# Optimization experiments

Hardware: AMD Instinct MI355X
Metric: run time of the kernel (lower is better)

The kernel has to match this reference:

```python
import jax, jax.numpy as jnp
import numpy as np

V = 12000; WE = 1000; FEAT = 2048; FE = 1024; H = 1024; AH = 512; NREG = 36; B = 128; T = 17
PAD_ID = 0


def _lstm_cell(x, h, c, wih, whh, bih, bhh):
    # torch LSTMCell: gates ordered (input, forget, cell, output)
    g = x @ wih.T + h @ whh.T + bih + bhh
    i, f, gg, o = jnp.split(g, 4, axis=-1)
    c_new = jax.nn.sigmoid(f) * c + jax.nn.sigmoid(i) * jnp.tanh(gg)
    h_new = jax.nn.sigmoid(o) * jnp.tanh(c_new)
    return h_new, c_new


def setup_inputs() -> dict:
    key = jax.random.key(0)
    ks = jax.random.split(key, 24)
    s = 0.02
    emb_w = jax.random.normal(ks[0], (V, WE), jnp.float32) * s
    emb_w = emb_w.at[PAD_ID].set(0.0)  # padding_idx row is zero
    inp = {
        'fc_feats': jax.random.normal(ks[1], (B, FEAT), jnp.float32),
        'att_feats': jax.random.normal(ks[2], (B, NREG, FEAT), jnp.float32),
        'captions': jax.random.randint(ks[3], (B, T), 0, V, jnp.int64),
        'emb_w': emb_w,
        'fc_w': jax.random.normal(ks[4], (FEAT, FE), jnp.float32) * s,
        'fc_b': jnp.zeros((FE,), jnp.float32),
        'atte_w': jax.random.normal(ks[5], (FEAT, FE), jnp.float32) * s,
        'atte_b': jnp.zeros((FE,), jnp.float32),
        'ctx_w': jax.random.normal(ks[6], (FE, AH), jnp.float32) * s,
        'ctx_b': jnp.zeros((AH,), jnp.float32),
        'attl_wih': jax.random.normal(ks[7], (4 * H, H + FE + WE), jnp.float32) * s,
        'attl_whh': jax.random.normal(ks[8], (4 * H, H), jnp.float32) * s,
        'attl_bih': jnp.zeros((4 * H,), jnp.float32),
        'attl_bhh': jnp.zeros((4 * H,), jnp.float32),
        'h2att_w': jax.random.normal(ks[9], (H, AH), jnp.float32) * s,
        'h2att_b': jnp.zeros((AH,), jnp.float32),
        'alpha_w': jax.random.normal(ks[10], (AH,), jnp.float32) * s,
        'alpha_b': jnp.zeros((), jnp.float32),
        'langl_wih': jax.random.normal(ks[11], (4 * H, FE + H), jnp.float32) * s,
        'langl_whh': jax.random.normal(ks[12], (4 * H, H), jnp.float32) * s,
        'langl_bih': jnp.zeros((4 * H,), jnp.float32),
        'langl_bhh': jnp.zeros((4 * H,), jnp.float32),
        'cls_w': jax.random.normal(ks[13], (H, V), jnp.float32) * s,
        'cls_b': jnp.zeros((V,), jnp.float32),
    }
    return inp


def _forward(fc_feats, att_feats, captions, emb_w, fc_w, fc_b, atte_w, atte_b,
             ctx_w, ctx_b, attl_wih, attl_whh, attl_bih, attl_bhh,
             h2att_w, h2att_b, alpha_w, alpha_b,
             langl_wih, langl_whh, langl_bih, langl_bhh, cls_w, cls_b):
    # _prepare_features (eval mode: dropout is identity)
    fc_e = jax.nn.relu(fc_feats @ fc_w + fc_b)                 # [B, FE]
    att_e = jax.nn.relu(att_feats @ atte_w + atte_b)           # [B, N, FE]
    p_att = att_e @ ctx_w + ctx_b                              # [B, N, AH]
    bsz = fc_feats.shape[0]
    h0 = jnp.zeros((bsz, H), fc_feats.dtype)

    def step(carry, it):
        h_att, c_att, h_lang, c_lang = carry
        w = jax.nn.relu(emb_w[it])                             # [B, WE]
        x_att = jnp.concatenate([h_lang, fc_e, w], axis=1)
        h_att, c_att = _lstm_cell(x_att, h_att, c_att, attl_wih, attl_whh, attl_bih, attl_bhh)
        # Attention
        hq = h_att @ h2att_w + h2att_b                          # [B, AH]
        e = jnp.tanh(p_att + hq[:, None, :]) @ alpha_w + alpha_b  # [B, N]
        alpha = jax.nn.softmax(e, axis=1)
        att_res = jnp.einsum('bn,bnd->bd', alpha, att_e)        # [B, FE]
        x_lang = jnp.concatenate([att_res, h_att], axis=1)
        h_lang, c_lang = _lstm_cell(x_lang, h_lang, c_lang, langl_wih, langl_whh, langl_bih, langl_bhh)
        logprobs = jax.nn.log_softmax(h_lang @ cls_w + cls_b, axis=1)  # [B, V]
        return (h_att, c_att, h_lang, c_lang), logprobs

    its = captions[:, :-1].T  # [T-1, B]
    _, outs = jax.lax.scan(step, (h0, h0, h0, h0), its)
    return jnp.transpose(outs, (1, 0, 2))  # [B, T-1, V]


def reference(fc_feats, att_feats, captions, emb_w, fc_w, fc_b, atte_w, atte_b,
              ctx_w, ctx_b, attl_wih, attl_whh, attl_bih, attl_bhh,
              h2att_w, h2att_b, alpha_w, alpha_b,
              langl_wih, langl_whh, langl_bih, langl_bhh, cls_w, cls_b):
    return _forward(fc_feats, att_feats, captions, emb_w, fc_w, fc_b, atte_w, atte_b,
                    ctx_w, ctx_b, attl_wih, attl_whh, attl_bih, attl_bhh,
                    h2att_w, h2att_b, alpha_w, alpha_b,
                    langl_wih, langl_whh, langl_bih, langl_bhh, cls_w, cls_b)
```

## Files before the change

kernel.cpp:

```cpp
#include <hip/hip_runtime.h>
#include <cstddef>
#include <cstdint>

constexpr int CV    = 12000;
constexpr int CVP2  = 12288;
constexpr int CWE   = 1000;
constexpr int CFEAT = 2048;
constexpr int CFE   = 1024;
constexpr int CH    = 1024;
constexpr int CAH   = 512;
constexpr int CNREG = 36;
constexpr int CB    = 128;
constexpr int CT    = 17;
constexpr int G4    = 4096;
constexpr int XH    = 2048;
constexpr int XL3   = 3072;

#define CDIV(a,b) (((a)+(b)-1)/(b))

typedef __bf16 bf16_t;
typedef __bf16 bf16x8 __attribute__((ext_vector_type(8)));
typedef __bf16 bf16x4 __attribute__((ext_vector_type(4)));
typedef float  f32x4  __attribute__((ext_vector_type(4)));

typedef __attribute__((address_space(3))) uint32_t lds_u32;
typedef const __attribute__((address_space(1))) uint32_t glb_u32;

struct Seg { const bf16_t* A; const bf16_t* W; int lda, ldw, kt; };

template<bool RELU, bool OUTBF, int SWZ>
__global__ __launch_bounds__(256)
void pre_gemm(Seg s0, int inner, const float* __restrict__ bias1,
              void* __restrict__ Cout, int ldc)
{
    const int tid = threadIdx.x;
    const int wid = tid >> 6, lane = tid & 63;
    const int wr = wid >> 1, wc = wid & 1;
    const int llo = lane & 15, lhi = lane >> 4;
    const int nb = gridDim.x, id = blockIdx.x;
    const int sw = (id & 7) * (nb >> 3) + (id >> 3);
    int m0, n0;
    if (SWZ == 1)      { n0 = (sw / inner) * 64;  m0 = (sw % inner) * 128; }
    else if (SWZ == 2) { m0 = (sw / inner) * 128; n0 = (sw % inner) * 64;  }
    else {
        const int xcd = id & 7, idx = id >> 3;
        m0 = (((xcd >> 2) << 3) + (idx & 7)) * 128;
        n0 = (((xcd & 3) << 4) + (idx >> 3)) * 64;
    }

    __shared__ __align__(16) uint8_t sm[2][24576];

    const int TT = s0.kt;
    f32x4 acc[4][2] = {};
    uint4 ra[4], rb[2];
    const int srow = tid >> 3, sc = tid & 7;
    const int cswz = (sc ^ (srow & 7)) << 4;

    auto load_tile = [&](int ti) {
        const int k0 = ti << 6;
        #pragma unroll
        for (int i = 0; i < 4; ++i)
            ra[i] = *(const uint4*)(s0.A + (size_t)(m0 + i * 32 + srow) * s0.lda + k0 + sc * 8);
        #pragma unroll
        for (int i = 0; i < 2; ++i)
            rb[i] = *(const uint4*)(s0.W + (size_t)(n0 + i * 32 + srow) * s0.ldw + k0 + sc * 8);
    };
    auto write_tile = [&](int buf) {
        uint8_t* base = sm[buf];
        #pragma unroll
        for (int i = 0; i < 4; ++i) *(uint4*)(base + (i * 32 + srow) * 128 + cswz) = ra[i];
        #pragma unroll
        for (int i = 0; i < 2; ++i) *(uint4*)(base + 16384 + (i * 32 + srow) * 128 + cswz) = rb[i];
    };
    auto compute = [&](int buf) {
        const uint8_t* base = sm[buf];
        const int r7 = llo & 7;
        #pragma unroll
        for (int kk = 0; kk < 2; ++kk) {
            const int coff = ((kk * 4 + lhi) ^ r7) << 4;
            bf16x8 af[4], bg[2];
            #pragma unroll
            for (int fm = 0; fm < 4; ++fm)
                af[fm] = *(const bf16x8*)(base + (wr * 64 + fm * 16 + llo) * 128 + coff);
            #pragma unroll
            for (int fn = 0; fn < 2; ++fn)
                bg[fn] = *(const bf16x8*)(base + 16384 + (wc * 32 + fn * 16 + llo) * 128 + coff);
            #pragma unroll
            for (int fm = 0; fm < 4; ++fm)
                #pragma unroll
                for (int fn = 0; fn < 2; ++fn)
                    acc[fm][fn] = __builtin_amdgcn_mfma_f32_16x16x32_bf16(
                        af[fm], bg[fn], acc[fm][fn], 0, 0, 0);
        }
    };

    load_tile(0); write_tile(0);
    load_tile(1);
    __syncthreads();
    int cur = 0;
    for (int ti = 0; ti < TT; ++ti) {
        if (ti + 1 < TT) write_tile(cur ^ 1);
        if (ti + 2 < TT) load_tile(ti + 2);
        compute(cur);
        __syncthreads();
        cur ^= 1;
    }

    if (OUTBF) {
        bf16_t* st = (bf16_t*)sm[0];
        #pragma unroll
        for (int fn = 0; fn < 2; ++fn) {
            const int lcol = wc * 32 + fn * 16 + llo;
            const float b = bias1 ? bias1[n0 + lcol] : 0.f;
            #pragma unroll
            for (int fm = 0; fm < 4; ++fm)
                #pragma unroll
                for (int r = 0; r < 4; ++r) {
                    float v = acc[fm][fn][r] + b;
                    if (RELU) v = fmaxf(v, 0.f);
                    st[(wr * 64 + fm * 16 + lhi * 4 + r) * 64 + lcol] = (bf16_t)v;
                }
        }
        __syncthreads();
        #pragma unroll
        for (int i = 0; i < 4; ++i) {
            const int q = tid + i * 256;
            const int row = q >> 3, ch = q & 7;
            *(uint4*)((bf16_t*)Cout + (size_t)(m0 + row) * ldc + n0 + ch * 8)
                = *(const uint4*)&st[row * 64 + ch * 8];
        }
    } else {
        const int colb = n0 + wc * 32;
        const int rowb = m0 + wr * 64 + lhi * 4;
        #pragma unroll
        for (int fn = 0; fn < 2; ++fn) {
            const int col = colb + fn * 16 + llo;
            const float b = bias1 ? bias1[col] : 0.f;
            #pragma unroll
            for (int fm = 0; fm < 4; ++fm)
                #pragma unroll
                for (int r = 0; r < 4; ++r) {
                    float v = acc[fm][fn][r] + b;
                    if (RELU) v = fmaxf(v, 0.f);
                    ((float*)Cout)[(size_t)(rowb + fm * 16 + r) * ldc + col] = v;
                }
        }
    }
}

__global__ __launch_bounds__(256)
void cls_gemm(const bf16_t* __restrict__ A, const bf16_t* __restrict__ W,
              const float* __restrict__ bias, bf16_t* __restrict__ Cout)
{
    const int tid = threadIdx.x;
    const int wid = tid >> 6, lane = tid & 63;
    const int wr = wid >> 1, wc = wid & 1;
    const int llo = lane & 15, lhi = lane >> 4;
    const int id = blockIdx.x;
    const int xcd = id & 7, idx = id >> 3;
    const int mg = xcd & 1, ng = xcd >> 1;
    const int m0 = (mg * 8 + (idx & 7)) * 128;
    const int n0 = (ng * 24 + (idx >> 3)) * 128;

    __shared__ __align__(16) uint8_t pool[65536];
    auto bufA = [&](int b) { return pool + b * 16384; };
    auto bufB = [&](int b) { return pool + 32768 + b * 16384; };

    constexpr int TT = 16;
    f32x4 acc[4][4] = {};
    uint4 ra[4], rbv[4];

    auto load_tile = [&](int ti) {
        const int k0 = ti << 6;
        #pragma unroll
        for (int i = 0; i < 4; ++i) {
            const int q = tid + i * 256;
            const int row = q >> 3, c = q & 7;
            ra[i]  = *(const uint4*)(A + (size_t)(m0 + row) * CH + k0 + c * 8);
            rbv[i] = *(const uint4*)(W + (size_t)(n0 + row) * CH + k0 + c * 8);
        }
    };
    auto write_tile = [&](int buf) {
        #pragma unroll
        for (int i = 0; i < 4; ++i) {
            const int q = tid + i * 256;
            const int row = q >> 3, c = q & 7;
            const int o = row * 128 + ((c ^ (row & 7)) << 4);
            *(uint4*)(bufA(buf) + o) = ra[i];
            *(uint4*)(bufB(buf) + o) = rbv[i];
        }
    };
    auto compute = [&](int buf) {
        const int r7 = llo & 7;
        #pragma unroll
        for (int kk = 0; kk < 2; ++kk) {
            const int coff = ((kk * 4 + lhi) ^ r7) << 4;
            bf16x8 af[4], bg[4];
            #pragma unroll
            for (int fm = 0; fm < 4; ++fm)
                af[fm] = *(const bf16x8*)(bufA(buf) + (wr * 64 + fm * 16 + llo) * 128 + coff);
            #pragma unroll
            for (int fn = 0; fn < 4; ++fn)
                bg[fn] = *(const bf16x8*)(bufB(buf) + (wc * 64 + fn * 16 + llo) * 128 + coff);
            #pragma unroll
            for (int fm = 0; fm < 4; ++fm)
                #pragma unroll
                for (int fn = 0; fn < 4; ++fn)
                    acc[fm][fn] = __builtin_amdgcn_mfma_f32_16x16x32_bf16(
                        af[fm], bg[fn], acc[fm][fn], 0, 0, 0);
        }
    };

    load_tile(0); write_tile(0);
    load_tile(1);
    __syncthreads();
    int cur = 0;
    for (int ti = 0; ti < TT; ++ti) {
        if (ti + 1 < TT) write_tile(cur ^ 1);
        if (ti + 2 < TT) load_tile(ti + 2);
        compute(cur);
        __syncthreads();
        cur ^= 1;
    }

    bf16_t* st = (bf16_t*)pool;
    #pragma unroll
    for (int fn = 0; fn < 4; ++fn) {
        const int lcol = wc * 64 + fn * 16 + llo;
        const int col = n0 + lcol;
        const float b = (col < CV) ? bias[col] : 0.f;
        #pragma unroll
        for (int fm = 0; fm < 4; ++fm)
            #pragma unroll
            for (int r = 0; r < 4; ++r)
                st[(wr * 64 + fm * 16 + lhi * 4 + r) * 128 + lcol]
                    = (bf16_t)(acc[fm][fn][r] + b);
    }
    __syncthreads();
    #pragma unroll
    for (int i = 0; i < 8; ++i) {
        const int q = tid + i * 256;
        const int row = q >> 4, ch = q & 15;
        *(uint4*)(Cout + (size_t)(m0 + row) * CVP2 + n0 + ch * 8)
            = *(const uint4*)&st[row * 128 + ch * 8];
    }
}

template<int TAG>
__global__ __launch_bounds__(256)
void gate_split(const bf16_t* __restrict__ A, int lda,
                const bf16_t* __restrict__ W, int ldw, int ktz,
                bf16_t* __restrict__ gpart)
{
    const int tid = threadIdx.x;
    const int w = tid >> 6, lane = tid & 63;
    const int llo = lane & 15, lhi = lane >> 4;
    const int n0 = blockIdx.x * 16;
    const int z  = blockIdx.y;
    const int kb = z * ktz;

    __shared__ __align__(16) uint8_t smA[2][16384];
    __shared__ __align__(16) uint8_t smB[2][2048];

    f32x4 acc0 = {0.f,0.f,0.f,0.f}, acc1 = {0.f,0.f,0.f,0.f};

    const int arow = tid >> 3, ac = tid & 7;
    const int asc = ac ^ (arow & 7);
    const int wvoff = (tid >> 6) * 1024;

    auto stage = [&](int buf, int ti) {
        const int k0 = (kb + ti) << 6;
        #pragma unroll
        for (int i = 0; i < 4; ++i) {
            const bf16_t* gp = A + (size_t)(arow + i * 32) * lda + k0 + asc * 8;
            __builtin_amdgcn_global_load_lds((glb_u32*)gp,
                (lds_u32*)(smA[buf] + i * 4096 + wvoff), 16, 0, 0);
        }
        if (tid < 128) {
            const int brow = tid >> 3, bc = tid & 7;
            const int bsc = bc ^ (brow & 7);
            const bf16_t* gp = W + (size_t)(n0 + brow) * ldw + k0 + bsc * 8;
            __builtin_amdgcn_global_load_lds((glb_u32*)gp,
                (lds_u32*)(smB[buf] + wvoff), 16, 0, 0);
        }
    };
    auto compute = [&](int buf) {
        const int r7 = llo & 7;
        #pragma unroll
        for (int kk = 0; kk < 2; ++kk) {
            const int coff = ((kk * 4 + lhi) ^ r7) << 4;
            bf16x8 a0 = *(const bf16x8*)(smA[buf] + (w * 32 + llo) * 128 + coff);
            bf16x8 a1 = *(const bf16x8*)(smA[buf] + (w * 32 + 16 + llo) * 128 + coff);
            bf16x8 bb = *(const bf16x8*)(smB[buf] + llo * 128 + coff);
            acc0 = __builtin_amdgcn_mfma_f32_16x16x32_bf16(a0, bb, acc0, 0, 0, 0);
            acc1 = __builtin_amdgcn_mfma_f32_16x16x32_bf16(a1, bb, acc1, 0, 0, 0);
        }
    };

    stage(0, 0);
    __syncthreads();
    int cur = 0;
    for (int ti = 0; ti < ktz; ++ti) {
        if (ti + 1 < ktz) stage(cur ^ 1, ti + 1);
        compute(cur);
        __syncthreads();
        cur ^= 1;
    }

    bf16_t* gp = gpart + (size_t)z * CB * G4;
    const int col = n0 + llo;
    #pragma unroll
    for (int r = 0; r < 4; ++r) {
        gp[(size_t)(w * 32 + lhi * 4 + r) * G4 + col] = (bf16_t)acc0[r];
        gp[(size_t)(w * 32 + 16 + lhi * 4 + r) * G4 + col] = (bf16_t)acc1[r];
    }
}

__global__ __launch_bounds__(1024)
void lstm_attn(const bf16_t* __restrict__ gpart, const bf16_t* __restrict__ gpre_fc,
               const bf16_t* __restrict__ gemb,
               const float* __restrict__ cbias, float* __restrict__ c_att,
               const bf16_t* __restrict__ p_att, const bf16_t* __restrict__ att_e,
               const bf16_t* __restrict__ h2att_wT, const float* __restrict__ h2att_b,
               const float* __restrict__ alpha_w, const float* __restrict__ alpha_b,
               bf16_t* __restrict__ xh_nxt, bf16_t* __restrict__ xl_cur)
{
    __shared__ float sh[CH];
    __shared__ float shq[CAH];
    __shared__ float se[64], salpha[64];
    const int b = blockIdx.x, tid = threadIdx.x;

    {
        const int j = tid;
        float g0 = 0.f, g1 = 0.f, g2 = 0.f, g3 = 0.f;
        #pragma unroll
        for (int z = 0; z < 4; ++z) {
            bf16x4 g = *(const bf16x4*)(gpart + (size_t)z * CB * G4 + (size_t)b * G4 + 4 * j);
            g0 += (float)g[0]; g1 += (float)g[1]; g2 += (float)g[2]; g3 += (float)g[3];
        }
        f32x4 cb = *(const f32x4*)(cbias + 4 * j);
        bf16x4 gf4 = *(const bf16x4*)(gpre_fc + (size_t)b * G4 + 4 * j);
        bf16x4 ge4 = *(const bf16x4*)(gemb + (size_t)b * G4 + 4 * j);
        const float gi = g0 + cb[0] + (float)gf4[0] + (float)ge4[0];
        const float gf = g1 + cb[1] + (float)gf4[1] + (float)ge4[1];
        const float gg = g2 + cb[2] + (float)gf4[2] + (float)ge4[2];
        const float go = g3 + cb[3] + (float)gf4[3] + (float)ge4[3];
        const float si = 1.f / (1.f + expf(-gi));
        const float sf = 1.f / (1.f + expf(-gf));
        const float so = 1.f / (1.f + expf(-go));
        const float cn = sf * c_att[b * CH + j] + si * tanhf(gg);
        const float hn = so * tanhf(cn);
        c_att[b * CH + j] = cn;
        sh[j] = hn;
        const bf16_t hb = (bf16_t)hn;
        xh_nxt[(size_t)b * XH + 1024 + j] = hb;
        xl_cur[(size_t)b * XL3 + 1024 + j] = hb;
    }
    __syncthreads();

    {
        const int q2 = tid & 1, n = tid >> 1;
        const bf16_t* wrow = h2att_wT + (size_t)n * CH + q2 * 512;
        float s = 0.f;
        #pragma unroll 4
        for (int k = 0; k < 512; k += 8) {
            bf16x8 w8 = *(const bf16x8*)(wrow + k);
            #pragma unroll
            for (int j = 0; j < 8; ++j) s = fmaf((float)w8[j], sh[q2 * 512 + k + j], s);
        }
        s += __shfl_xor(s, 1);
        if (q2 == 0) shq[n] = s + h2att_b[n];
    }
    __syncthreads();

    {
        const int wave = tid >> 6, lane = tid & 63;
        for (int n = wave; n < CNREG; n += 16) {
            const bf16_t* pr = p_att + ((size_t)b * CNREG + n) * CAH;
            float s = 0.f;
            #pragma unroll
            for (int q = 0; q < CAH / 64; ++q) {
                const int d = lane + q * 64;
                s += alpha_w[d] * tanhf((float)pr[d] + shq[d]);
            }
            for (int off = 32; off; off >>= 1) s += __shfl_down(s, off);
            if (lane == 0) se[n] = s + alpha_b[0];
        }
    }
    __syncthreads();

    {
        float mx = -1e30f;
        for (int n = 0; n < CNREG; ++n) mx = fmaxf(mx, se[n]);
        float sum = 0.f;
        for (int n = 0; n < CNREG; ++n) sum += expf(se[n] - mx);
        if (tid < CNREG) salpha[tid] = expf(se[tid] - mx) / sum;
    }
    __syncthreads();

    {
        const int d = tid;
        float s = 0.f;
        const bf16_t* ae = att_e + (size_t)b * CNREG * CFE + d;
        #pragma unroll 4
        for (int n = 0; n < CNREG; ++n)
            s = fmaf(salpha[n], (float)ae[(size_t)n * CFE], s);
        xl_cur[(size_t)b * XL3 + d] = (bf16_t)s;
    }
}

__global__ __launch_bounds__(256)
void lstm_flat(const bf16_t* __restrict__ gpart, const float* __restrict__ cbias,
               float* __restrict__ c,
               bf16_t* __restrict__ xh_nxt, bf16_t* __restrict__ xl_nxt,
               bf16_t* __restrict__ h_all, int t)
{
    const int idx = blockIdx.x * 256 + threadIdx.x;
    const int b = idx >> 10, j = idx & 1023;
    float g0 = 0.f, g1 = 0.f, g2 = 0.f, g3 = 0.f;
    #pragma unroll
    for (int z = 0; z < 4; ++z) {
        bf16x4 g = *(const bf16x4*)(gpart + (size_t)z * CB * G4 + (size_t)b * G4 + 4 * j);
        g0 += (float)g[0]; g1 += (float)g[1]; g2 += (float)g[2]; g3 += (float)g[3];
    }
    f32x4 cb = *(const f32x4*)(cbias + 4 * j);
    const float si = 1.f / (1.f + expf(-(g0 + cb[0])));
    const float sf = 1.f / (1.f + expf(-(g1 + cb[1])));
    const float so = 1.f / (1.f + expf(-(g3 + cb[3])));
    const float cn = sf * c[idx] + si * tanhf(g2 + cb[2]);
    const float hn = so * tanhf(cn);
    c[idx] = cn;
    const bf16_t hb = (bf16_t)hn;
    xh_nxt[(size_t)b * XH + j] = hb;
    xl_nxt[(size_t)b * XL3 + 2048 + j] = hb;
    h_all[((size_t)b * (CT - 1) + t) * CH + j] = hb;
}

__global__ void convert_pad(const float* __restrict__ src, bf16_t* __restrict__ dst,
                            int C, int Cp)
{
    const int r = blockIdx.y;
    const int c = blockIdx.x * 256 + threadIdx.x;
    if (c >= Cp) return;
    dst[(size_t)r * Cp + c] = (c < C) ? (bf16_t)src[(size_t)r * C + c] : (bf16_t)0.f;
}

__global__ void convert_perm(const float* __restrict__ src, int srcld, int scol0,
                             int valid, bf16_t* __restrict__ dst, int dstld, int dcol0,
                             int ncols)
{
    const int rp = blockIdx.y;
    const int c = blockIdx.x * 256 + threadIdx.x;
    if (c >= ncols) return;
    const int rs = (rp & 3) * 1024 + (rp >> 2);
    const float v = (c < valid) ? src[(size_t)rs * srcld + scol0 + c] : 0.f;
    dst[(size_t)rp * dstld + dcol0 + c] = (bf16_t)v;
}

__global__ void bias_perm(const float* __restrict__ bih, const float* __restrict__ bhh,
                          float* __restrict__ dst)
{
    const int rp = blockIdx.x * 256 + threadIdx.x;
    if (rp >= G4) return;
    const int rs = (rp & 3) * 1024 + (rp >> 2);
    dst[rp] = bih[rs] + bhh[rs];
}

__global__ __launch_bounds__(256)
void transpose_convert(const float* __restrict__ src, bf16_t* __restrict__ dst,
                       int K, int N)
{
    __shared__ float tile[32][33];
    const int n0 = blockIdx.x * 32, k0 = blockIdx.y * 32;
    const int tx = threadIdx.x & 31, ty = threadIdx.x >> 5;
    #pragma unroll
    for (int i = 0; i < 4; ++i) {
        const int k = k0 + ty + i * 8, n = n0 + tx;
        tile[ty + i * 8][tx] = (k < K && n < N) ? src[(size_t)k * N + n] : 0.f;
    }
    __syncthreads();
    #pragma unroll
    for (int i = 0; i < 4; ++i) {
        const int n = n0 + ty + i * 8, k = k0 + tx;
        if (n < N && k < K) dst[(size_t)n * K + k] = (bf16_t)tile[tx][ty + i * 8];
    }
}

__global__ void emb_all(const float* __restrict__ emb_w,
                        const int* __restrict__ captions, bf16_t* __restrict__ w_emb)
{
    const int r = blockIdx.y;
    const int j = blockIdx.x * 256 + threadIdx.x;
    const int t = r >> 7, b = r & 127;
    const int tok = captions[b * CT + t];
    const float v = (j < CWE) ? fmaxf(emb_w[(size_t)tok * CWE + j], 0.f) : 0.f;
    w_emb[(size_t)r * 1024 + j] = (bf16_t)v;
}

__global__ __launch_bounds__(256)
void logsoftmax_bf(const bf16_t* __restrict__ lg, float* __restrict__ out)
{
    __shared__ float red[4];
    const int r = blockIdx.x, tid = threadIdx.x;
    const bf16_t* row = lg + (size_t)r * CVP2;

    float v[48];
    float mx = -1e30f;
    #pragma unroll
    for (int i = 0; i < 6; ++i) {
        const int c = tid + i * 256;
        if (c < 1500) {
            bf16x8 x = *(const bf16x8*)(row + c * 8);
            #pragma unroll
            for (int j = 0; j < 8; ++j) {
                v[i * 8 + j] = (float)x[j];
                mx = fmaxf(mx, v[i * 8 + j]);
            }
        } else {
            #pragma unroll
            for (int j = 0; j < 8; ++j) v[i * 8 + j] = -1e30f;
        }
    }
    for (int off = 32; off; off >>= 1) mx = fmaxf(mx, __shfl_down(mx, off));
    if ((tid & 63) == 0) red[tid >> 6] = mx;
    __syncthreads();
    mx = fmaxf(fmaxf(red[0], red[1]), fmaxf(red[2], red[3]));
    __syncthreads();

    float sum = 0.f;
    #pragma unroll
    for (int i = 0; i < 6; ++i)
        if (tid + i * 256 < 1500)
            #pragma unroll
            for (int j = 0; j < 8; ++j) sum += expf(v[i * 8 + j] - mx);
    for (int off = 32; off; off >>= 1) sum += __shfl_down(sum, off);
    if ((tid & 63) == 0) red[tid >> 6] = sum;
    __syncthreads();
    sum = red[0] + red[1] + red[2] + red[3];
    const float lse = mx + logf(sum);

    #pragma unroll
    for (int i = 0; i < 6; ++i) {
        const int c = tid + i * 256;
        if (c < 1500) {
            float* o = out + (size_t)r * CV + c * 8;
            float4 a = make_float4(v[i*8+0]-lse, v[i*8+1]-lse, v[i*8+2]-lse, v[i*8+3]-lse);
            float4 bq = make_float4(v[i*8+4]-lse, v[i*8+5]-lse, v[i*8+6]-lse, v[i*8+7]-lse);
            *(float4*)o = a;
            *(float4*)(o + 4) = bq;
        }
    }
}

extern "C" void kernel_launch(void* const* d_in, const int* in_sizes, int n_in,
                              void* d_out, int out_size, void* d_ws, size_t ws_size,
                              hipStream_t stream)
{
    const float* fc_feats  = (const float*)d_in[0];
    const float* att_feats = (const float*)d_in[1];
    const int*   captions  = (const int*)  d_in[2];
    const float* emb_w     = (const float*)d_in[3];
    const float* fc_w      = (const float*)d_in[4];
    const float* fc_b      = (const float*)d_in[5];
    const float* atte_w    = (const float*)d_in[6];
    const float* atte_b    = (const float*)d_in[7];
    const float* ctx_w     = (const float*)d_in[8];
    const float* ctx_b     = (const float*)d_in[9];
    const float* attl_wih  = (const float*)d_in[10];
    const float* attl_whh  = (const float*)d_in[11];
    const float* attl_bih  = (const float*)d_in[12];
    const float* attl_bhh  = (const float*)d_in[13];
    const float* h2att_w   = (const float*)d_in[14];
    const float* h2att_b   = (const float*)d_in[15];
    const float* alpha_w   = (const float*)d_in[16];
    const float* alpha_b   = (const float*)d_in[17];
    const float* langl_wih = (const float*)d_in[18];
    const float* langl_whh = (const float*)d_in[19];
    const float* langl_bih = (const float*)d_in[20];
    const float* langl_bhh = (const float*)d_in[21];
    const float* cls_w     = (const float*)d_in[22];
    const float* cls_b     = (const float*)d_in[23];

    float* out = (float*)d_out;

    char* p = (char*)d_ws;
    auto alloc_bf = [&](size_t e) { bf16_t* q = (bf16_t*)p; p += e * 2; return q; };
    auto alloc_f  = [&](size_t e) { float*  q = (float*) p; p += e * 4; return q; };

    bf16_t* Wcat_att    = alloc_bf((size_t)G4 * XH);
    bf16_t* Wcat_lang   = alloc_bf((size_t)G4 * XL3);
    bf16_t* Win_fc      = alloc_bf((size_t)G4 * 1024);
    bf16_t* Win_emb     = alloc_bf((size_t)G4 * 1024);
    bf16_t* fc_wT_b     = alloc_bf((size_t)CFE * CFEAT);
    bf16_t* atte_wT_b   = alloc_bf((size_t)CFE * CFEAT);
    bf16_t* ctx_wT_b    = alloc_bf((size_t)CAH * CFE);
    bf16_t* h2att_wT_b  = alloc_bf((size_t)CAH * CH);
    bf16_t* cls_wT_b    = alloc_bf((size_t)CVP2 * CH);
    bf16_t* fc_feats_b  = alloc_bf((size_t)CB * CFEAT);
    bf16_t* att_feats_b = alloc_bf((size_t)CB * CNREG * CFEAT);
    bf16_t* att_e_b     = alloc_bf((size_t)CB * CNREG * CFE);
    bf16_t* w_emb       = alloc_bf((size_t)(CT - 1) * CB * 1024);
    bf16_t* fc_e_b      = alloc_bf((size_t)CB * CFE);
    bf16_t* gpre_fc     = alloc_bf((size_t)CB * G4);
    bf16_t* xh0         = alloc_bf((size_t)CB * XH);
    bf16_t* xh1         = alloc_bf((size_t)CB * XH);
    bf16_t* xl3a        = alloc_bf((size_t)CB * XL3);
    bf16_t* xl3b        = alloc_bf((size_t)CB * XL3);
    bf16_t* h_all       = alloc_bf((size_t)CB * (CT - 1) * CH);
    bf16_t* p_att       = alloc_bf((size_t)CB * CNREG * CAH);
    bf16_t* gpart       = alloc_bf((size_t)4 * CB * G4);
    float*  cbias_att   = alloc_f (G4);
    float*  cbias_lang  = alloc_f (G4);
    float*  c_att       = alloc_f ((size_t)CB * CH);
    float*  c_lang      = alloc_f ((size_t)CB * CH);

    bf16_t* Gemb   = att_feats_b;
    bf16_t* logits = Wcat_att;

    hipMemsetAsync(xh0,    0, (size_t)CB * XH * 2, stream);
    hipMemsetAsync(xh1,    0, (size_t)CB * XH * 2, stream);
    hipMemsetAsync(xl3a,   0, (size_t)CB * XL3 * 2, stream);
    hipMemsetAsync(xl3b,   0, (size_t)CB * XL3 * 2, stream);
    hipMemsetAsync(c_att,  0, (size_t)CB * CH * 4, stream);
    hipMemsetAsync(c_lang, 0, (size_t)CB * CH * 4, stream);
    hipMemsetAsync(cls_wT_b + (size_t)CV * CH, 0, (size_t)(CVP2 - CV) * CH * 2, stream);

    const dim3 blk(256);
    auto mk = [](const bf16_t* A, int lda, const bf16_t* W, int ldw, int kt) {
        return Seg{A, W, lda, ldw, kt};
    };

    convert_perm<<<dim3(4, G4), blk, 0, stream>>>(attl_wih, 3048, 0, 1024, Wcat_att, XH, 0, 1024);
    convert_perm<<<dim3(4, G4), blk, 0, stream>>>(attl_whh, 1024, 0, 1024, Wcat_att, XH, 1024, 1024);
    convert_perm<<<dim3(4, G4), blk, 0, stream>>>(attl_wih, 3048, 1024, 1024, Win_fc, 1024, 0, 1024);
    convert_perm<<<dim3(4, G4), blk, 0, stream>>>(attl_wih, 3048, 2048, 1000, Win_emb, 1024, 0, 1024);
    convert_perm<<<dim3(8, G4), blk, 0, stream>>>(langl_wih, 2048, 0, 2048, Wcat_lang, XL3, 0, 2048);
    convert_perm<<<dim3(4, G4), blk, 0, stream>>>(langl_whh, 1024, 0, 1024, Wcat_lang, XL3, 2048, 1024);
    bias_perm<<<16, blk, 0, stream>>>(attl_bih, attl_bhh, cbias_att);
    bias_perm<<<16, blk, 0, stream>>>(langl_bih, langl_bhh, cbias_lang);
    convert_pad<<<dim3(8, CB), blk, 0, stream>>>(fc_feats, fc_feats_b, CFEAT, CFEAT);
    convert_pad<<<dim3(8, CB * CNREG), blk, 0, stream>>>(att_feats, att_feats_b, CFEAT, CFEAT);
    transpose_convert<<<dim3(CFE/32, CFEAT/32), blk, 0, stream>>>(fc_w,    fc_wT_b,    CFEAT, CFE);
    transpose_convert<<<dim3(CFE/32, CFEAT/32), blk, 0, stream>>>(atte_w,  atte_wT_b,  CFEAT, CFE);
    transpose_convert<<<dim3(CAH/32, CFE/32),   blk, 0, stream>>>(ctx_w,   ctx_wT_b,   CFE,   CAH);
    transpose_convert<<<dim3(CAH/32, CH/32),    blk, 0, stream>>>(h2att_w, h2att_wT_b, CH,    CAH);
    transpose_convert<<<dim3(CDIV(CV,32), CH/32), blk, 0, stream>>>(cls_w, cls_wT_b,   CH,    CV);
    emb_all<<<dim3(4, (CT - 1) * CB), blk, 0, stream>>>(emb_w, captions, w_emb);

    pre_gemm<true,true,2><<<16, blk, 0, stream>>>(
        mk(fc_feats_b, CFEAT, fc_wT_b, CFEAT, 32), 16, fc_b, fc_e_b, CFE);
    pre_gemm<true,true,2><<<576, blk, 0, stream>>>(
        mk(att_feats_b, CFEAT, atte_wT_b, CFEAT, 32), 16, atte_b, att_e_b, CFE);
    pre_gemm<false,true,2><<<288, blk, 0, stream>>>(
        mk(att_e_b, CFE, ctx_wT_b, CFE, 16), 8, ctx_b, p_att, CAH);
    pre_gemm<false,true,1><<<64, blk, 0, stream>>>(
        mk(fc_e_b, CFE, Win_fc, 1024, 16), 1, nullptr, gpre_fc, G4);
    pre_gemm<false,true,3><<<1024, blk, 0, stream>>>(
        mk(w_emb, 1024, Win_emb, 1024, 16), 0, nullptr, Gemb, G4);

    for (int t = 0; t < CT - 1; ++t) {
        bf16_t* xh_cur = (t & 1) ? xh1 : xh0;
        bf16_t* xh_nxt = (t & 1) ? xh0 : xh1;
        bf16_t* xl_cur = (t & 1) ? xl3b : xl3a;
        bf16_t* xl_nxt = (t & 1) ? xl3a : xl3b;

        gate_split<0><<<dim3(256, 4), blk, 0, stream>>>(
            xh_cur, XH, Wcat_att, XH, 8, gpart);

        lstm_attn<<<CB, dim3(1024), 0, stream>>>(
            gpart, gpre_fc, Gemb + (size_t)t * CB * G4, cbias_att, c_att,
            p_att, att_e_b, h2att_wT_b, h2att_b, alpha_w, alpha_b,
            xh_nxt, xl_cur);

        gate_split<1><<<dim3(256, 4), blk, 0, stream>>>(
            xl_cur, XL3, Wcat_lang, XL3, 12, gpart);

        lstm_flat<<<512, blk, 0, stream>>>(
            gpart, cbias_lang, c_lang, xh_nxt, xl_nxt, h_all, t);
    }

    cls_gemm<<<1536, blk, 0, stream>>>(h_all, cls_wT_b, cls_b, logits);
    logsoftmax_bf<<<2048, blk, 0, stream>>>(logits, out);
}
```

Before: 1.909 ms.

## Give each wave private LDS tiles in gate_split and drop block barriers

gate_split now gives every wave its own slice of LDS holding its 32 A rows plus a private copy of the 16-row W tile. Each wave then only waits on its own async global-to-LDS loads with s_waitcnt vmcnt instead of __syncthreads, and it prefetches two tiles ahead. The cost is that the W tile is loaded four times per block, and correctness relies on the hand-written vmcnt counts matching the number of issued loads. Separately, the classifier epilogue staging buffer gets a padded row stride of 136 to reduce LDS bank conflicts.

```diff
diff --git a/kernel.cpp b/kernel.cpp
--- a/kernel.cpp
+++ b/kernel.cpp
@@ -223,6 +223,7 @@
         cur ^= 1;
     }
 
+    constexpr int STR = 136;
     bf16_t* st = (bf16_t*)pool;
     #pragma unroll
     for (int fn = 0; fn < 4; ++fn) {
@@ -233,7 +234,7 @@
         for (int fm = 0; fm < 4; ++fm)
             #pragma unroll
             for (int r = 0; r < 4; ++r)
-                st[(wr * 64 + fm * 16 + lhi * 4 + r) * 128 + lcol]
+                st[(wr * 64 + fm * 16 + lhi * 4 + r) * STR + lcol]
                     = (bf16_t)(acc[fm][fn][r] + b);
     }
     __syncthreads();
@@ -242,7 +243,7 @@
         const int q = tid + i * 256;
         const int row = q >> 4, ch = q & 15;
         *(uint4*)(Cout + (size_t)(m0 + row) * CVP2 + n0 + ch * 8)
-            = *(const uint4*)&st[row * 128 + ch * 8];
+            = *(const uint4*)&st[row * STR + ch * 8];
     }
 }
 
@@ -259,51 +260,56 @@
     const int z  = blockIdx.y;
     const int kb = z * ktz;
 
-    __shared__ __align__(16) uint8_t smA[2][16384];
-    __shared__ __align__(16) uint8_t smB[2][2048];
+    __shared__ __align__(16) uint8_t sm[4][2][6144];
 
     f32x4 acc0 = {0.f,0.f,0.f,0.f}, acc1 = {0.f,0.f,0.f,0.f};
-
-    const int arow = tid >> 3, ac = tid & 7;
-    const int asc = ac ^ (arow & 7);
-    const int wvoff = (tid >> 6) * 1024;
 
     auto stage = [&](int buf, int ti) {
         const int k0 = (kb + ti) << 6;
+        uint8_t* base = sm[w][buf];
         #pragma unroll
         for (int i = 0; i < 4; ++i) {
-            const bf16_t* gp = A + (size_t)(arow + i * 32) * lda + k0 + asc * 8;
+            const int q = lane + i * 64;
+            const int row = q >> 3, c = q & 7;
+            const int scz = c ^ (row & 7);
+            const bf16_t* gp = A + (size_t)(w * 32 + row) * lda + k0 + scz * 8;
             __builtin_amdgcn_global_load_lds((glb_u32*)gp,
-                (lds_u32*)(smA[buf] + i * 4096 + wvoff), 16, 0, 0);
-        }
-        if (tid < 128) {
-            const int brow = tid >> 3, bc = tid & 7;
-            const int bsc = bc ^ (brow & 7);
-            const bf16_t* gp = W + (size_t)(n0 + brow) * ldw + k0 + bsc * 8;
+                (lds_u32*)(base + i * 1024 + lane * 16), 16, 0, 0);
+        }
+        #pragma unroll
+        for (int i = 0; i < 2; ++i) {
+            const int q = lane + i * 64;
+            const int row = q >> 3, c = q & 7;
+            const int scz = c ^ (row & 7);
+            const bf16_t* gp = W + (size_t)(n0 + row) * ldw + k0 + scz * 8;
             __builtin_amdgcn_global_load_lds((glb_u32*)gp,
-                (lds_u32*)(smB[buf] + wvoff), 16, 0, 0);
+                (lds_u32*)(base + 4096 + i * 1024 + lane * 16), 16, 0, 0);
         }
     };
     auto compute = [&](int buf) {
+        const uint8_t* base = sm[w][buf];
         const int r7 = llo & 7;
         #pragma unroll
         for (int kk = 0; kk < 2; ++kk) {
             const int coff = ((kk * 4 + lhi) ^ r7) << 4;
-            bf16x8 a0 = *(const bf16x8*)(smA[buf] + (w * 32 + llo) * 128 + coff);
-            bf16x8 a1 = *(const bf16x8*)(smA[buf] + (w * 32 + 16 + llo) * 128 + coff);
-            bf16x8 bb = *(const bf16x8*)(smB[buf] + llo * 128 + coff);
+            bf16x8 a0 = *(const bf16x8*)(base + llo * 128 + coff);
+            bf16x8 a1 = *(const bf16x8*)(base + (16 + llo) * 128 + coff);
+            bf16x8 bb = *(const bf16x8*)(base + 4096 + llo * 128 + coff);
             acc0 = __builtin_amdgcn_mfma_f32_16x16x32_bf16(a0, bb, acc0, 0, 0, 0);
             acc1 = __builtin_amdgcn_mfma_f32_16x16x32_bf16(a1, bb, acc1, 0, 0, 0);
         }
     };
 
     stage(0, 0);
-    __syncthreads();
+    if (ktz > 1) stage(1, 1);
     int cur = 0;
     for (int ti = 0; ti < ktz; ++ti) {
-        if (ti + 1 < ktz) stage(cur ^ 1, ti + 1);
+        if (ti + 1 < ktz) asm volatile("s_waitcnt vmcnt(6)" ::: "memory");
+        else              asm volatile("s_waitcnt vmcnt(0)" ::: "memory");
+        __builtin_amdgcn_sched_barrier(0);
         compute(cur);
-        __syncthreads();
+        __builtin_amdgcn_sched_barrier(0);
+        if (ti + 2 < ktz) stage(cur, ti + 2);
         cur ^= 1;
     }
 
```

Result: no change. 1.918 ms (+0.5%).
